# Optimization experiments

Hardware: AMD Instinct MI355X
Metric: run time of the kernel (lower is better)

## Reference

```python
import jax, jax.numpy as jnp
import numpy as np

EMBED, MID = 2048, 256
SLOPE = 0.2

def _lrelu(v):
    return jnp.where(v >= 0, v, SLOPE * v)

def setup_inputs() -> dict:
    key = jax.random.key(0)
    ks = jax.random.split(key, 9)
    B, C, L = 4, EMBED, 4096
    s_in = 1.0 / np.sqrt(C)
    s_mid = 1.0 / np.sqrt(MID)
    return {
        "x":   jax.random.normal(ks[0], (B, C, L), dtype=jnp.float32),
        "W_t": jax.random.uniform(ks[1], (MID, C), jnp.float32, -s_in, s_in),
        "b_t": jax.random.uniform(ks[2], (MID,), jnp.float32, -s_in, s_in),
        "W_p": jax.random.uniform(ks[3], (MID, C), jnp.float32, -s_in, s_in),
        "b_p": jax.random.uniform(ks[4], (MID,), jnp.float32, -s_in, s_in),
        "W_g": jax.random.uniform(ks[5], (MID, C), jnp.float32, -s_in, s_in),
        "b_g": jax.random.uniform(ks[6], (MID,), jnp.float32, -s_in, s_in),
        "W_o": jax.random.uniform(ks[7], (C, MID), jnp.float32, -s_mid, s_mid),
        "b_o": jax.random.uniform(ks[8], (C,), jnp.float32, -s_mid, s_mid),
    }

def reference(x, W_t, b_t, W_p, b_p, W_g, b_g, W_o, b_o):
    # x: [B, C, L]; 1x1 conv == channel matmul. Dropout is identity (eval mode).
    theta = _lrelu(jnp.einsum('mc,bcl->bml', W_t, x) + b_t[None, :, None])  # [B, M, L]
    phi   = _lrelu(jnp.einsum('mc,bcl->bml', W_p, x) + b_p[None, :, None])  # [B, M, L]
    gamma = _lrelu(jnp.einsum('mc,bcl->bml', W_g, x) + b_g[None, :, None])  # [B, M, L]
    # scores: phi^T @ theta -> [B, L, L], fixed scale 1/32
    scores = jnp.einsum('bmi,bmj->bij', phi, theta) / 32.0
    attn = jax.nn.softmax(scores, axis=-1)
    # y: attn @ gamma^T -> [B, L, M], then back to [B, M, L]
    y = jnp.einsum('bij,bmj->bmi', attn, gamma)
    out = x + _lrelu(jnp.einsum('cm,bml->bcl', W_o, y) + b_o[None, :, None])
    return out
```

## Files before the change

### kernel.cpp

```cpp
#include <hip/hip_runtime.h>
#include <stdint.h>

#define B_ 4
#define C_ 2048
#define L_ 4096
#define M_ 256
#define M3_ 768
#define SLOPE_ 0.2f
#define SPLIT_ 4
#define KVB_ 32

typedef __attribute__((ext_vector_type(8))) short short8;
typedef __attribute__((ext_vector_type(4))) float f32x4;

__device__ __forceinline__ unsigned short f2bf(float f) {
    union { float f; unsigned u; } v; v.f = f;
    unsigned r = v.u + 0x7FFF + ((v.u >> 16) & 1);
    return (unsigned short)(r >> 16);
}
__device__ __forceinline__ unsigned short f2bf_rz(float f) {
    union { float f; unsigned u; } v; v.f = f;
    return (unsigned short)(v.u >> 16);
}
__device__ __forceinline__ unsigned pack2(float a, float b) {
    return (unsigned)f2bf(a) | ((unsigned)f2bf(b) << 16);
}
__device__ __forceinline__ float lrelu(float v) { return v >= 0.f ? v : SLOPE_ * v; }

__device__ __forceinline__ void gload_lds16(const void* g, void* l) {
    __builtin_amdgcn_global_load_lds(
        (const __attribute__((address_space(1))) void*)g,
        (__attribute__((address_space(3))) void*)l, 16, 0, 0);
}

__global__ __launch_bounds__(256) void prep_x(
    const float* __restrict__ x, unsigned short* __restrict__ xT)
{
    const int l = blockIdx.x * 64 + (threadIdx.x & 63);
    const int c = blockIdx.y * 32 + (threadIdx.x >> 6) * 8;
    const int b = blockIdx.z;
    const float* src = x + ((size_t)b * C_ + c) * L_ + l;
    unsigned v[4];
    #pragma unroll
    for (int j = 0; j < 4; ++j)
        v[j] = pack2(src[(size_t)(2 * j) * L_], src[(size_t)(2 * j + 1) * L_]);
    *reinterpret_cast<uint4*>(&xT[((size_t)b * L_ + l) * C_ + c]) =
        *reinterpret_cast<uint4*>(v);
}

__global__ __launch_bounds__(256) void prep_w(
    const float* __restrict__ Wt, const float* __restrict__ Wp,
    const float* __restrict__ Wg, const float* __restrict__ Wo,
    unsigned short* __restrict__ w3, unsigned short* __restrict__ wo)
{
    const size_t NW = (size_t)M_ * C_;
    size_t e = ((size_t)blockIdx.x * 256 + threadIdx.x) * 8;
    const float* src; unsigned short* dst;
    if (e < NW)          { src = Wt + e;          dst = w3 + e; }
    else if (e < 2 * NW) { src = Wp + (e - NW);   dst = w3 + e; }
    else if (e < 3 * NW) { src = Wg + (e - 2*NW); dst = w3 + e; }
    else                 { src = Wo + (e - 3*NW); dst = wo + (e - 3*NW); }
    float4 a = *reinterpret_cast<const float4*>(src);
    float4 b = *reinterpret_cast<const float4*>(src + 4);
    unsigned v[4] = { pack2(a.x, a.y), pack2(a.z, a.w),
                      pack2(b.x, b.y), pack2(b.z, b.w) };
    *reinterpret_cast<uint4*>(dst) = *reinterpret_cast<uint4*>(v);
}

__global__ __launch_bounds__(256, 3) void proj_kernel(
    const unsigned short* __restrict__ w3,
    const float* __restrict__ bt, const float* __restrict__ bp,
    const float* __restrict__ bg,
    const unsigned short* __restrict__ xT,
    unsigned short* __restrict__ theta,
    unsigned short* __restrict__ phi,
    unsigned short* __restrict__ gammaT)
{
    __shared__ unsigned short As[128 * 64];
    __shared__ unsigned short Bs[128 * 64];

    const int l0 = blockIdx.x * 128;
    const int m0 = blockIdx.y * 128;
    const int b  = blockIdx.z;
    const int t  = threadIdx.x;
    const int wave = t >> 6, lane = t & 63;
    const int lr = lane & 15, lg = lane >> 4;
    const int wm = (wave >> 1) * 64, wl = (wave & 1) * 64;

    const int which = m0 >> 8;
    const float* bsrc = (which == 0) ? bt : (which == 1) ? bp : bg;
    const int mw = m0 & 255;

    const unsigned short* abase = w3 + (size_t)m0 * C_;
    const unsigned short* bbase = xT + ((size_t)b * L_ + l0) * C_;

    const int srow = lane >> 3;
    const int scol = ((lane & 7) ^ srow) * 8;

    f32x4 acc[4][4] = {};

    for (int k0 = 0; k0 < C_; k0 += 64) {
        __syncthreads();
        #pragma unroll
        for (int i = 0; i < 4; ++i) {
            int chunk = wave * 4 + i;
            int row = chunk * 8 + srow;
            gload_lds16(abase + (size_t)row * C_ + k0 + scol, As + chunk * 512);
            gload_lds16(bbase + (size_t)row * C_ + k0 + scol, Bs + chunk * 512);
        }
        __syncthreads();

        #pragma unroll
        for (int ks = 0; ks < 2; ++ks) {
            short8 af[4], bf[4];
            #pragma unroll
            for (int mi = 0; mi < 4; ++mi)
                af[mi] = *reinterpret_cast<const short8*>(
                    &As[(wm + mi * 16 + lr) * 64 +
                        ((ks * 32 + lg * 8) ^ ((lr & 7) << 3))]);
            #pragma unroll
            for (int ni = 0; ni < 4; ++ni)
                bf[ni] = *reinterpret_cast<const short8*>(
                    &Bs[(wl + ni * 16 + lr) * 64 +
                        ((ks * 32 + lg * 8) ^ ((lr & 7) << 3))]);
            #pragma unroll
            for (int mi = 0; mi < 4; ++mi)
                #pragma unroll
                for (int ni = 0; ni < 4; ++ni)
                    acc[mi][ni] = __builtin_amdgcn_mfma_f32_16x16x32_bf16(
                        af[mi], bf[ni], acc[mi][ni], 0, 0, 0);
        }
    }

    if (which < 2) {
        unsigned short* dst = (which == 0) ? theta : phi;
        const float scale = (which == 1) ? 0.03125f : 1.0f;
        #pragma unroll
        for (int mi = 0; mi < 4; ++mi) {
            const int mloc = mw + wm + mi * 16 + lg * 4;
            float b0 = bsrc[mloc], b1 = bsrc[mloc + 1];
            float b2 = bsrc[mloc + 2], b3 = bsrc[mloc + 3];
            #pragma unroll
            for (int ni = 0; ni < 4; ++ni) {
                int l = l0 + wl + ni * 16 + lr;
                uint2 pk;
                pk.x = pack2(lrelu(acc[mi][ni][0] + b0) * scale,
                             lrelu(acc[mi][ni][1] + b1) * scale);
                pk.y = pack2(lrelu(acc[mi][ni][2] + b2) * scale,
                             lrelu(acc[mi][ni][3] + b3) * scale);
                *reinterpret_cast<uint2*>(&dst[((size_t)b * L_ + l) * M_ + mloc]) = pk;
            }
        }
    } else {
        #pragma unroll
        for (int mi = 0; mi < 4; ++mi) {
            #pragma unroll
            for (int r = 0; r < 4; ++r) {
                int m = mw + wm + mi * 16 + lg * 4 + r;
                float bias = bsrc[m];
                #pragma unroll
                for (int ni = 0; ni < 4; ++ni) {
                    int l = l0 + wl + ni * 16 + lr;
                    gammaT[((size_t)b * M_ + m) * L_ + l] =
                        f2bf(lrelu(acc[mi][ni][r] + bias));
                }
            }
        }
    }
}

__global__ __launch_bounds__(512, 1) void attn_kernel(
    const unsigned short* __restrict__ phi,
    const unsigned short* __restrict__ theta,
    const unsigned short* __restrict__ gammaT,
    float* __restrict__ yp,
    float* __restrict__ rsp)
{
    __shared__ unsigned short Ks[2][KVB_ * 256];
    __shared__ unsigned short Vs[2][256 * KVB_];
    __shared__ unsigned short Ps[8][32][42];

    const int q0 = blockIdx.x * 256;
    const int s  = blockIdx.y;
    const int b  = blockIdx.z;
    const int kvbase = s * (L_ / SPLIT_);
    const int t  = threadIdx.x;
    const int wave = t >> 6, lane = t & 63;
    const int lr = lane & 15, lg = lane >> 4;

    const unsigned short* theta_b = theta  + (size_t)b * L_ * M_;
    const unsigned short* gamma_b = gammaT + (size_t)b * M_ * L_;

    short8 qf[2][8];
    #pragma unroll
    for (int u = 0; u < 2; ++u) {
        const unsigned short* qrow =
            phi + ((size_t)b * L_ + q0 + wave * 32 + u * 16 + lr) * M_ + lg * 8;
        #pragma unroll
        for (int ks = 0; ks < 8; ++ks)
            qf[u][ks] = *reinterpret_cast<const short8*>(qrow + ks * 32);
    }

    f32x4 accy[2][16] = {};
    float rsum[2][4] = {};

    auto stage_k = [&](unsigned short* buf, int kv0) {
        #pragma unroll
        for (int q = 0; q < 2; ++q) {
            int c   = q * 512 + t;
            int row = c >> 5;
            int cb  = (c & 31) << 4;
            int cbs = cb ^ ((row & 7) << 4);
            const unsigned short* src = theta_b + (size_t)(kv0 + row) * M_ + (cbs >> 1);
            unsigned short* ldst = buf + ((size_t)(q * 512 + wave * 64) << 3);
            gload_lds16(src, ldst);
        }
    };
    auto stage_v = [&](unsigned short* buf, int kv0) {
        #pragma unroll
        for (int q = 0; q < 2; ++q) {
            int c  = q * 512 + t;
            int mh = c >> 3;
            int tb = ((c & 7) << 4) ^ ((mh & 7) << 4);
            int m  = mh * 2 + (tb >> 6);
            int j  = (tb & 63) >> 1;
            const unsigned short* src = gamma_b + (size_t)m * L_ + kv0 + j;
            unsigned short* ldst = buf + ((size_t)(q * 512 + wave * 64) << 3);
            gload_lds16(src, ldst);
        }
    };

    stage_k(&Ks[0][0], kvbase);
    stage_v(&Vs[0][0], kvbase);
    __syncthreads();

    int cur = 0;
    for (int it = 0; it < L_ / SPLIT_ / KVB_; ++it) {
        if (it + 1 < L_ / SPLIT_ / KVB_) {
            stage_k(&Ks[cur ^ 1][0], kvbase + (it + 1) * KVB_);
            stage_v(&Vs[cur ^ 1][0], kvbase + (it + 1) * KVB_);
        }

        f32x4 sacc[2][2] = {};
        __builtin_amdgcn_s_setprio(1);
        #pragma unroll
        for (int ks = 0; ks < 8; ++ks) {
            #pragma unroll
            for (int jt = 0; jt < 2; ++jt) {
                int jr = jt * 16 + lr;
                int cbl = ks * 64 + lg * 16;
                short8 bf = *reinterpret_cast<const short8*>(
                    &Ks[cur][jr * 256 + (((cbl ^ ((jr & 7) << 4)) >> 1))]);
                sacc[0][jt] = __builtin_amdgcn_mfma_f32_16x16x32_bf16(qf[0][ks], bf, sacc[0][jt], 0, 0, 0);
                sacc[1][jt] = __builtin_amdgcn_mfma_f32_16x16x32_bf16(qf[1][ks], bf, sacc[1][jt], 0, 0, 0);
            }
        }
        __builtin_amdgcn_s_setprio(0);

        #pragma unroll
        for (int u = 0; u < 2; ++u)
            #pragma unroll
            for (int jt = 0; jt < 2; ++jt)
                #pragma unroll
                for (int r = 0; r < 4; ++r) {
                    float p = __expf(sacc[u][jt][r]);
                    rsum[u][r] += p;
                    Ps[wave][u * 16 + lg * 4 + r][lr + 16 * jt] = f2bf_rz(p);
                }

        short8 paf[2];
        paf[0] = *reinterpret_cast<const short8*>(&Ps[wave][lr][lg * 8]);
        paf[1] = *reinterpret_cast<const short8*>(&Ps[wave][16 + lr][lg * 8]);
        __builtin_amdgcn_s_setprio(1);
        #pragma unroll
        for (int mt = 0; mt < 16; ++mt) {
            int m = mt * 16 + lr;
            int byte = (m >> 1) * 128 +
                       ((((m & 1) * 64 + lg * 16)) ^ (((m >> 1) & 7) << 4));
            short8 bf = *reinterpret_cast<const short8*>(&Vs[cur][byte >> 1]);
            accy[0][mt] = __builtin_amdgcn_mfma_f32_16x16x32_bf16(paf[0], bf, accy[0][mt], 0, 0, 0);
            accy[1][mt] = __builtin_amdgcn_mfma_f32_16x16x32_bf16(paf[1], bf, accy[1][mt], 0, 0, 0);
        }
        __builtin_amdgcn_s_setprio(0);

        __syncthreads();
        cur ^= 1;
    }

    float* ypb = yp + (((size_t)(s * B_ + b) * L_) + q0) * M_;
    #pragma unroll
    for (int u = 0; u < 2; ++u)
        #pragma unroll
        for (int r = 0; r < 4; ++r) {
            int row = wave * 32 + u * 16 + lg * 4 + r;
            #pragma unroll
            for (int mt = 0; mt < 16; ++mt)
                ypb[(size_t)row * M_ + lr + 16 * mt] = accy[u][mt][r];
            float ssum = rsum[u][r];
            #pragma unroll
            for (int off = 1; off < 16; off <<= 1)
                ssum += __shfl_xor(ssum, off, 64);
            if (lr == 0)
                rsp[((size_t)(s * B_ + b) * L_) + q0 + row] = ssum;
        }
}

__global__ __launch_bounds__(256) void reduce_kernel(
    const float* __restrict__ yp,
    const float* __restrict__ rsp,
    unsigned short* __restrict__ y)
{
    const int idx = blockIdx.x * 256 + threadIdx.x;
    const int ml  = (idx * 8) & (M_ - 1);
    const int row = (idx * 8) >> 8;
    const int b   = row >> 12;
    const int l   = row & (L_ - 1);

    float acc[8] = {};
    float rs = 0.f;
    #pragma unroll
    for (int s = 0; s < SPLIT_; ++s) {
        const float* p = yp + (((size_t)(s * B_ + b) * L_) + l) * M_ + ml;
        float4 a = *reinterpret_cast<const float4*>(p);
        float4 c = *reinterpret_cast<const float4*>(p + 4);
        acc[0] += a.x; acc[1] += a.y; acc[2] += a.z; acc[3] += a.w;
        acc[4] += c.x; acc[5] += c.y; acc[6] += c.z; acc[7] += c.w;
        rs += rsp[((size_t)(s * B_ + b) * L_) + l];
    }
    float inv = 1.f / rs;
    unsigned v[4] = { pack2(acc[0] * inv, acc[1] * inv),
                      pack2(acc[2] * inv, acc[3] * inv),
                      pack2(acc[4] * inv, acc[5] * inv),
                      pack2(acc[6] * inv, acc[7] * inv) };
    *reinterpret_cast<uint4*>(&y[((size_t)b * L_ + l) * M_ + ml]) =
        *reinterpret_cast<uint4*>(v);
}

__global__ __launch_bounds__(256, 3) void out_kernel(
    const float* __restrict__ x,
    const unsigned short* __restrict__ wo,
    const float* __restrict__ bo,
    const unsigned short* __restrict__ y,
    float* __restrict__ out)
{
    __shared__ unsigned short As[128 * 64];
    __shared__ unsigned short Bs[128 * 64];

    const int l0 = blockIdx.x * 128;
    const int c0 = blockIdx.y * 128;
    const int b  = blockIdx.z;
    const int t  = threadIdx.x;
    const int wave = t >> 6, lane = t & 63;
    const int lr = lane & 15, lg = lane >> 4;
    const int wm = (wave >> 1) * 64, wl = (wave & 1) * 64;

    const unsigned short* abase = wo + (size_t)c0 * M_;
    const unsigned short* bbase = y + ((size_t)b * L_ + l0) * M_;

    const int srow = lane >> 3;
    const int scol = ((lane & 7) ^ srow) * 8;

    f32x4 acc[4][4] = {};

    for (int k0 = 0; k0 < M_; k0 += 64) {
        __syncthreads();
        #pragma unroll
        for (int i = 0; i < 4; ++i) {
            int chunk = wave * 4 + i;
            int row = chunk * 8 + srow;
            gload_lds16(abase + (size_t)row * M_ + k0 + scol, As + chunk * 512);
            gload_lds16(bbase + (size_t)row * M_ + k0 + scol, Bs + chunk * 512);
        }
        __syncthreads();

        #pragma unroll
        for (int ks = 0; ks < 2; ++ks) {
            short8 af[4], bf[4];
            #pragma unroll
            for (int mi = 0; mi < 4; ++mi)
                af[mi] = *reinterpret_cast<const short8*>(
                    &As[(wm + mi * 16 + lr) * 64 +
                        ((ks * 32 + lg * 8) ^ ((lr & 7) << 3))]);
            #pragma unroll
            for (int ni = 0; ni < 4; ++ni)
                bf[ni] = *reinterpret_cast<const short8*>(
                    &Bs[(wl + ni * 16 + lr) * 64 +
                        ((ks * 32 + lg * 8) ^ ((lr & 7) << 3))]);
            #pragma unroll
            for (int mi = 0; mi < 4; ++mi)
                #pragma unroll
                for (int ni = 0; ni < 4; ++ni)
                    acc[mi][ni] = __builtin_amdgcn_mfma_f32_16x16x32_bf16(
                        af[mi], bf[ni], acc[mi][ni], 0, 0, 0);
        }
    }

    #pragma unroll
    for (int mi = 0; mi < 4; ++mi) {
        #pragma unroll
        for (int r = 0; r < 4; ++r) {
            int c = c0 + wm + mi * 16 + lg * 4 + r;
            float bias = bo[c];
            #pragma unroll
            for (int ni = 0; ni < 4; ++ni) {
                int l = l0 + wl + ni * 16 + lr;
                size_t idx = ((size_t)b * C_ + c) * L_ + l;
                out[idx] = x[idx] + lrelu(acc[mi][ni][r] + bias);
            }
        }
    }
}

extern "C" void kernel_launch(void* const* d_in, const int* in_sizes, int n_in,
                              void* d_out, int out_size, void* d_ws, size_t ws_size,
                              hipStream_t stream) {
    const float* x  = (const float*)d_in[0];
    const float* Wt = (const float*)d_in[1];
    const float* bt = (const float*)d_in[2];
    const float* Wp = (const float*)d_in[3];
    const float* bp = (const float*)d_in[4];
    const float* Wg = (const float*)d_in[5];
    const float* bg = (const float*)d_in[6];
    const float* Wo = (const float*)d_in[7];
    const float* bo = (const float*)d_in[8];
    float* out = (float*)d_out;

    unsigned short* xT    = (unsigned short*)d_ws;
    unsigned short* w3    = xT + (size_t)B_ * L_ * C_;
    unsigned short* wob   = w3 + (size_t)M3_ * C_;
    unsigned short* theta = wob + (size_t)C_ * M_;
    unsigned short* phi   = theta + (size_t)B_ * L_ * M_;
    unsigned short* gammaT= phi   + (size_t)B_ * L_ * M_;

    float* yp  = (float*)xT;
    float* rsp = (float*)w3;
    unsigned short* yb = theta;

    prep_x<<<dim3(L_ / 64, C_ / 32, B_), 256, 0, stream>>>(x, xT);
    prep_w<<<dim3(2097152 / 8 / 256), 256, 0, stream>>>(Wt, Wp, Wg, Wo, w3, wob);
    proj_kernel<<<dim3(L_ / 128, M3_ / 128, B_), 256, 0, stream>>>(
        w3, bt, bp, bg, xT, theta, phi, gammaT);
    attn_kernel<<<dim3(L_ / 256, SPLIT_, B_), 512, 0, stream>>>(
        phi, theta, gammaT, yp, rsp);
    reduce_kernel<<<dim3((B_ * L_ * M_ / 8) / 256), 256, 0, stream>>>(yp, rsp, yb);
    out_kernel<<<dim3(L_ / 128, C_ / 128, B_), 256, 0, stream>>>(x, wob, bo, yb, out);
}
```

Baseline: 269.5 us.

## Split attention work across 16 waves with 16 query rows each

```diff
diff --git a/kernel.cpp b/kernel.cpp
--- a/kernel.cpp
+++ b/kernel.cpp
@@ -169,7 +169,7 @@
     }
 }
 
-__global__ __launch_bounds__(512, 1) void attn_kernel(
+__global__ __launch_bounds__(1024, 4) void attn_kernel(
     const unsigned short* __restrict__ phi,
     const unsigned short* __restrict__ theta,
     const unsigned short* __restrict__ gammaT,
@@ -178,7 +178,7 @@
 {
     __shared__ unsigned short Ks[2][KVB_ * 256];
     __shared__ unsigned short Vs[2][256 * KVB_];
-    __shared__ unsigned short Ps[8][32][42];
+    __shared__ unsigned short Ps[16][16][42];
 
     const int q0 = blockIdx.x * 256;
     const int s  = blockIdx.y;
@@ -191,47 +191,37 @@
     const unsigned short* theta_b = theta  + (size_t)b * L_ * M_;
     const unsigned short* gamma_b = gammaT + (size_t)b * M_ * L_;
 
-    short8 qf[2][8];
-    #pragma unroll
-    for (int u = 0; u < 2; ++u) {
-        const unsigned short* qrow =
-            phi + ((size_t)b * L_ + q0 + wave * 32 + u * 16 + lr) * M_ + lg * 8;
-        #pragma unroll
-        for (int ks = 0; ks < 8; ++ks)
-            qf[u][ks] = *reinterpret_cast<const short8*>(qrow + ks * 32);
-    }
-
-    f32x4 accy[2][16] = {};
-    float rsum[2][4] = {};
-
     auto stage_k = [&](unsigned short* buf, int kv0) {
-        #pragma unroll
-        for (int q = 0; q < 2; ++q) {
-            int c   = q * 512 + t;
-            int row = c >> 5;
-            int cb  = (c & 31) << 4;
-            int cbs = cb ^ ((row & 7) << 4);
-            const unsigned short* src = theta_b + (size_t)(kv0 + row) * M_ + (cbs >> 1);
-            unsigned short* ldst = buf + ((size_t)(q * 512 + wave * 64) << 3);
-            gload_lds16(src, ldst);
-        }
+        int row = t >> 5;
+        int cb  = (t & 31) << 4;
+        int cbs = cb ^ ((row & 7) << 4);
+        const unsigned short* src = theta_b + (size_t)(kv0 + row) * M_ + (cbs >> 1);
+        gload_lds16(src, buf + ((size_t)(wave * 64) << 3));
     };
     auto stage_v = [&](unsigned short* buf, int kv0) {
-        #pragma unroll
-        for (int q = 0; q < 2; ++q) {
-            int c  = q * 512 + t;
-            int mh = c >> 3;
-            int tb = ((c & 7) << 4) ^ ((mh & 7) << 4);
-            int m  = mh * 2 + (tb >> 6);
-            int j  = (tb & 63) >> 1;
-            const unsigned short* src = gamma_b + (size_t)m * L_ + kv0 + j;
-            unsigned short* ldst = buf + ((size_t)(q * 512 + wave * 64) << 3);
-            gload_lds16(src, ldst);
-        }
+        int mh = t >> 3;
+        int tb = ((t & 7) << 4) ^ ((mh & 7) << 4);
+        int m  = mh * 2 + (tb >> 6);
+        int j  = (tb & 63) >> 1;
+        const unsigned short* src = gamma_b + (size_t)m * L_ + kv0 + j;
+        gload_lds16(src, buf + ((size_t)(wave * 64) << 3));
     };
 
     stage_k(&Ks[0][0], kvbase);
     stage_v(&Vs[0][0], kvbase);
+
+    short8 qf[8];
+    {
+        const unsigned short* qrow =
+            phi + ((size_t)b * L_ + q0 + wave * 16 + lr) * M_ + lg * 8;
+        #pragma unroll
+        for (int ks = 0; ks < 8; ++ks)
+            qf[ks] = *reinterpret_cast<const short8*>(qrow + ks * 32);
+    }
+
+    f32x4 accy[16] = {};
+    float rsum[4] = {};
+
     __syncthreads();
 
     int cur = 0;
@@ -241,7 +231,7 @@
             stage_v(&Vs[cur ^ 1][0], kvbase + (it + 1) * KVB_);
         }
 
-        f32x4 sacc[2][2] = {};
+        f32x4 sacc[2] = {};
         __builtin_amdgcn_s_setprio(1);
         #pragma unroll
         for (int ks = 0; ks < 8; ++ks) {
@@ -251,26 +241,21 @@
                 int cbl = ks * 64 + lg * 16;
                 short8 bf = *reinterpret_cast<const short8*>(
                     &Ks[cur][jr * 256 + (((cbl ^ ((jr & 7) << 4)) >> 1))]);
-                sacc[0][jt] = __builtin_amdgcn_mfma_f32_16x16x32_bf16(qf[0][ks], bf, sacc[0][jt], 0, 0, 0);
-                sacc[1][jt] = __builtin_amdgcn_mfma_f32_16x16x32_bf16(qf[1][ks], bf, sacc[1][jt], 0, 0, 0);
+                sacc[jt] = __builtin_amdgcn_mfma_f32_16x16x32_bf16(qf[ks], bf, sacc[jt], 0, 0, 0);
             }
         }
         __builtin_amdgcn_s_setprio(0);
 
         #pragma unroll
-        for (int u = 0; u < 2; ++u)
-            #pragma unroll
-            for (int jt = 0; jt < 2; ++jt)
-                #pragma unroll
-                for (int r = 0; r < 4; ++r) {
-                    float p = __expf(sacc[u][jt][r]);
-                    rsum[u][r] += p;
-                    Ps[wave][u * 16 + lg * 4 + r][lr + 16 * jt] = f2bf_rz(p);
-                }
-
-        short8 paf[2];
-        paf[0] = *reinterpret_cast<const short8*>(&Ps[wave][lr][lg * 8]);
-        paf[1] = *reinterpret_cast<const short8*>(&Ps[wave][16 + lr][lg * 8]);
+        for (int jt = 0; jt < 2; ++jt)
+            #pragma unroll
+            for (int r = 0; r < 4; ++r) {
+                float p = __expf(sacc[jt][r]);
+                rsum[r] += p;
+                Ps[wave][lg * 4 + r][lr + 16 * jt] = f2bf_rz(p);
+            }
+
+        short8 paf = *reinterpret_cast<const short8*>(&Ps[wave][lr][lg * 8]);
         __builtin_amdgcn_s_setprio(1);
         #pragma unroll
         for (int mt = 0; mt < 16; ++mt) {
@@ -278,8 +263,7 @@
             int byte = (m >> 1) * 128 +
                        ((((m & 1) * 64 + lg * 16)) ^ (((m >> 1) & 7) << 4));
             short8 bf = *reinterpret_cast<const short8*>(&Vs[cur][byte >> 1]);
-            accy[0][mt] = __builtin_amdgcn_mfma_f32_16x16x32_bf16(paf[0], bf, accy[0][mt], 0, 0, 0);
-            accy[1][mt] = __builtin_amdgcn_mfma_f32_16x16x32_bf16(paf[1], bf, accy[1][mt], 0, 0, 0);
+            accy[mt] = __builtin_amdgcn_mfma_f32_16x16x32_bf16(paf, bf, accy[mt], 0, 0, 0);
         }
         __builtin_amdgcn_s_setprio(0);
 
@@ -289,20 +273,18 @@
 
     float* ypb = yp + (((size_t)(s * B_ + b) * L_) + q0) * M_;
     #pragma unroll
-    for (int u = 0; u < 2; ++u)
-        #pragma unroll
-        for (int r = 0; r < 4; ++r) {
-            int row = wave * 32 + u * 16 + lg * 4 + r;
-            #pragma unroll
-            for (int mt = 0; mt < 16; ++mt)
-                ypb[(size_t)row * M_ + lr + 16 * mt] = accy[u][mt][r];
-            float ssum = rsum[u][r];
-            #pragma unroll
-            for (int off = 1; off < 16; off <<= 1)
-                ssum += __shfl_xor(ssum, off, 64);
-            if (lr == 0)
-                rsp[((size_t)(s * B_ + b) * L_) + q0 + row] = ssum;
-        }
+    for (int r = 0; r < 4; ++r) {
+        int row = wave * 16 + lg * 4 + r;
+        #pragma unroll
+        for (int mt = 0; mt < 16; ++mt)
+            ypb[(size_t)row * M_ + lr + 16 * mt] = accy[mt][r];
+        float ssum = rsum[r];
+        #pragma unroll
+        for (int off = 1; off < 16; off <<= 1)
+            ssum += __shfl_xor(ssum, off, 64);
+        if (lr == 0)
+            rsp[((size_t)(s * B_ + b) * L_) + q0 + row] = ssum;
+    }
 }
 
 __global__ __launch_bounds__(256) void reduce_kernel(
@@ -440,7 +422,7 @@
     prep_w<<<dim3(2097152 / 8 / 256), 256, 0, stream>>>(Wt, Wp, Wg, Wo, w3, wob);
     proj_kernel<<<dim3(L_ / 128, M3_ / 128, B_), 256, 0, stream>>>(
         w3, bt, bp, bg, xT, theta, phi, gammaT);
-    attn_kernel<<<dim3(L_ / 256, SPLIT_, B_), 512, 0, stream>>>(
+    attn_kernel<<<dim3(L_ / 256, SPLIT_, B_), 1024, 0, stream>>>(
         phi, theta, gammaT, yp, rsp);
     reduce_kernel<<<dim3((B_ * L_ * M_ / 8) / 256), 256, 0, stream>>>(yp, rsp, yb);
     out_kernel<<<dim3(L_ / 128, C_ / 128, B_), 256, 0, stream>>>(x, wob, bo, yb, out);
```

Result: slower. 289.3 us (+7.3%).

## Shrink attention blocks to 256 threads, single-buffer KV, store partials as bf16

Applied to the files above, without the earlier changes.

```diff
diff --git a/kernel.cpp b/kernel.cpp
--- a/kernel.cpp
+++ b/kernel.cpp
@@ -24,6 +24,9 @@
 }
 __device__ __forceinline__ unsigned pack2(float a, float b) {
     return (unsigned)f2bf(a) | ((unsigned)f2bf(b) << 16);
+}
+__device__ __forceinline__ float bf2f(unsigned short u) {
+    union { unsigned u; float f; } v; v.u = (unsigned)u << 16; return v.f;
 }
 __device__ __forceinline__ float lrelu(float v) { return v >= 0.f ? v : SLOPE_ * v; }
 
@@ -169,18 +172,18 @@
     }
 }
 
-__global__ __launch_bounds__(512, 1) void attn_kernel(
+__global__ __launch_bounds__(256, 2) void attn_kernel(
     const unsigned short* __restrict__ phi,
     const unsigned short* __restrict__ theta,
     const unsigned short* __restrict__ gammaT,
-    float* __restrict__ yp,
+    unsigned short* __restrict__ yp,
     float* __restrict__ rsp)
 {
-    __shared__ unsigned short Ks[2][KVB_ * 256];
-    __shared__ unsigned short Vs[2][256 * KVB_];
-    __shared__ unsigned short Ps[8][32][42];
-
-    const int q0 = blockIdx.x * 256;
+    __shared__ unsigned short Ks[KVB_ * 256];
+    __shared__ unsigned short Vs[256 * KVB_];
+    __shared__ unsigned short Ps[4][32][42];
+
+    const int q0 = blockIdx.x * 128;
     const int s  = blockIdx.y;
     const int b  = blockIdx.z;
     const int kvbase = s * (L_ / SPLIT_);
@@ -195,7 +198,7 @@
     #pragma unroll
     for (int u = 0; u < 2; ++u) {
         const unsigned short* qrow =
-            phi + ((size_t)b * L_ + q0 + wave * 32 + u * 16 + lr) * M_ + lg * 8;
+            phi + ((size_t)b * L_ + q0 + u * 64 + wave * 16 + lr) * M_ + lg * 8;
         #pragma unroll
         for (int ks = 0; ks < 8; ++ks)
             qf[u][ks] = *reinterpret_cast<const short8*>(qrow + ks * 32);
@@ -204,42 +207,35 @@
     f32x4 accy[2][16] = {};
     float rsum[2][4] = {};
 
-    auto stage_k = [&](unsigned short* buf, int kv0) {
-        #pragma unroll
-        for (int q = 0; q < 2; ++q) {
-            int c   = q * 512 + t;
+    auto stage_k = [&](int kv0) {
+        #pragma unroll
+        for (int q = 0; q < 4; ++q) {
+            int c   = q * 256 + wave * 64 + lane;
             int row = c >> 5;
             int cb  = (c & 31) << 4;
             int cbs = cb ^ ((row & 7) << 4);
             const unsigned short* src = theta_b + (size_t)(kv0 + row) * M_ + (cbs >> 1);
-            unsigned short* ldst = buf + ((size_t)(q * 512 + wave * 64) << 3);
-            gload_lds16(src, ldst);
+            gload_lds16(src, &Ks[0] + ((size_t)(q * 256 + wave * 64) << 3));
         }
     };
-    auto stage_v = [&](unsigned short* buf, int kv0) {
-        #pragma unroll
-        for (int q = 0; q < 2; ++q) {
-            int c  = q * 512 + t;
+    auto stage_v = [&](int kv0) {
+        #pragma unroll
+        for (int q = 0; q < 4; ++q) {
+            int c  = q * 256 + wave * 64 + lane;
             int mh = c >> 3;
             int tb = ((c & 7) << 4) ^ ((mh & 7) << 4);
             int m  = mh * 2 + (tb >> 6);
             int j  = (tb & 63) >> 1;
             const unsigned short* src = gamma_b + (size_t)m * L_ + kv0 + j;
-            unsigned short* ldst = buf + ((size_t)(q * 512 + wave * 64) << 3);
-            gload_lds16(src, ldst);
+            gload_lds16(src, &Vs[0] + ((size_t)(q * 256 + wave * 64) << 3));
         }
     };
 
-    stage_k(&Ks[0][0], kvbase);
-    stage_v(&Vs[0][0], kvbase);
-    __syncthreads();
-
-    int cur = 0;
     for (int it = 0; it < L_ / SPLIT_ / KVB_; ++it) {
-        if (it + 1 < L_ / SPLIT_ / KVB_) {
-            stage_k(&Ks[cur ^ 1][0], kvbase + (it + 1) * KVB_);
-            stage_v(&Vs[cur ^ 1][0], kvbase + (it + 1) * KVB_);
-        }
+        __syncthreads();
+        stage_k(kvbase + it * KVB_);
+        stage_v(kvbase + it * KVB_);
+        __syncthreads();
 
         f32x4 sacc[2][2] = {};
         __builtin_amdgcn_s_setprio(1);
@@ -250,7 +246,7 @@
                 int jr = jt * 16 + lr;
                 int cbl = ks * 64 + lg * 16;
                 short8 bf = *reinterpret_cast<const short8*>(
-                    &Ks[cur][jr * 256 + (((cbl ^ ((jr & 7) << 4)) >> 1))]);
+                    &Ks[jr * 256 + (((cbl ^ ((jr & 7) << 4)) >> 1))]);
                 sacc[0][jt] = __builtin_amdgcn_mfma_f32_16x16x32_bf16(qf[0][ks], bf, sacc[0][jt], 0, 0, 0);
                 sacc[1][jt] = __builtin_amdgcn_mfma_f32_16x16x32_bf16(qf[1][ks], bf, sacc[1][jt], 0, 0, 0);
             }
@@ -277,25 +273,22 @@
             int m = mt * 16 + lr;
             int byte = (m >> 1) * 128 +
                        ((((m & 1) * 64 + lg * 16)) ^ (((m >> 1) & 7) << 4));
-            short8 bf = *reinterpret_cast<const short8*>(&Vs[cur][byte >> 1]);
+            short8 bf = *reinterpret_cast<const short8*>(&Vs[byte >> 1]);
             accy[0][mt] = __builtin_amdgcn_mfma_f32_16x16x32_bf16(paf[0], bf, accy[0][mt], 0, 0, 0);
             accy[1][mt] = __builtin_amdgcn_mfma_f32_16x16x32_bf16(paf[1], bf, accy[1][mt], 0, 0, 0);
         }
         __builtin_amdgcn_s_setprio(0);
-
-        __syncthreads();
-        cur ^= 1;
-    }
-
-    float* ypb = yp + (((size_t)(s * B_ + b) * L_) + q0) * M_;
+    }
+
+    unsigned short* ypb = yp + (((size_t)(s * B_ + b) * L_) + q0) * M_;
     #pragma unroll
     for (int u = 0; u < 2; ++u)
         #pragma unroll
         for (int r = 0; r < 4; ++r) {
-            int row = wave * 32 + u * 16 + lg * 4 + r;
+            int row = u * 64 + wave * 16 + lg * 4 + r;
             #pragma unroll
             for (int mt = 0; mt < 16; ++mt)
-                ypb[(size_t)row * M_ + lr + 16 * mt] = accy[u][mt][r];
+                ypb[(size_t)row * M_ + lr + 16 * mt] = f2bf(accy[u][mt][r]);
             float ssum = rsum[u][r];
             #pragma unroll
             for (int off = 1; off < 16; off <<= 1)
@@ -306,7 +299,7 @@
 }
 
 __global__ __launch_bounds__(256) void reduce_kernel(
-    const float* __restrict__ yp,
+    const unsigned short* __restrict__ yp,
     const float* __restrict__ rsp,
     unsigned short* __restrict__ y)
 {
@@ -320,11 +313,14 @@
     float rs = 0.f;
     #pragma unroll
     for (int s = 0; s < SPLIT_; ++s) {
-        const float* p = yp + (((size_t)(s * B_ + b) * L_) + l) * M_ + ml;
-        float4 a = *reinterpret_cast<const float4*>(p);
-        float4 c = *reinterpret_cast<const float4*>(p + 4);
-        acc[0] += a.x; acc[1] += a.y; acc[2] += a.z; acc[3] += a.w;
-        acc[4] += c.x; acc[5] += c.y; acc[6] += c.z; acc[7] += c.w;
+        uint4 raw = *reinterpret_cast<const uint4*>(
+            &yp[(((size_t)(s * B_ + b) * L_) + l) * M_ + ml]);
+        const unsigned* dw = reinterpret_cast<const unsigned*>(&raw);
+        #pragma unroll
+        for (int k = 0; k < 4; ++k) {
+            acc[2 * k]     += bf2f((unsigned short)(dw[k] & 0xFFFF));
+            acc[2 * k + 1] += bf2f((unsigned short)(dw[k] >> 16));
+        }
         rs += rsp[((size_t)(s * B_ + b) * L_) + l];
     }
     float inv = 1.f / rs;
@@ -432,7 +428,7 @@
     unsigned short* phi   = theta + (size_t)B_ * L_ * M_;
     unsigned short* gammaT= phi   + (size_t)B_ * L_ * M_;
 
-    float* yp  = (float*)xT;
+    unsigned short* yp = xT;
     float* rsp = (float*)w3;
     unsigned short* yb = theta;
 
@@ -440,7 +436,7 @@
     prep_w<<<dim3(2097152 / 8 / 256), 256, 0, stream>>>(Wt, Wp, Wg, Wo, w3, wob);
     proj_kernel<<<dim3(L_ / 128, M3_ / 128, B_), 256, 0, stream>>>(
         w3, bt, bp, bg, xT, theta, phi, gammaT);
-    attn_kernel<<<dim3(L_ / 256, SPLIT_, B_), 512, 0, stream>>>(
+    attn_kernel<<<dim3(L_ / 128, SPLIT_, B_), 256, 0, stream>>>(
         phi, theta, gammaT, yp, rsp);
     reduce_kernel<<<dim3((B_ * L_ * M_ / 8) / 256), 256, 0, stream>>>(yp, rsp, yb);
     out_kernel<<<dim3(L_ / 128, C_ / 128, B_), 256, 0, stream>>>(x, wob, bo, yb, out);
```

Measured after the change: 274.4 us. Within noise of the previous version (+1.8%).
